# Kernel tuning notes

Measured on AMD Instinct MI355X. Metric: run time of the kernel, lower is better.

## Reference

```python
import jax, jax.numpy as jnp
import numpy as np

T, B = 128, 4096
TB = T * B
NUM_ACTIONS, N_WORDS, EMB = 6, 16, 16
IMG_FEAT, LOC_DIM, HID = 16, 4, 128
IN_DIM = IMG_FEAT + LOC_DIM + EMB  # 36
GRID_SIZE = 5.0


def setup_inputs() -> dict:
    key = jax.random.key(0)
    ks = jax.random.split(key, 32)
    p = lambda i, shape, s=0.1: (jax.random.normal(ks[i], shape, dtype=jnp.float32) * s)
    inp = {
        'image': jax.random.uniform(ks[0], (TB, 1, 3, 3), dtype=jnp.float32) * 255.0,
        'location': jax.random.uniform(ks[1], (TB, 2), dtype=jnp.float32) * GRID_SIZE,
        'message': jax.random.randint(ks[2], (TB,), 0, N_WORDS, dtype=jnp.int32),
        'done': (jax.random.uniform(ks[3], (TB,)) < 0.05).astype(jnp.float32),
        'h0': p(4, (B, HID)),
        'c0': p(5, (B, HID)),
        # visual encoder 9->256->256->128->16
        'vw1': p(6, (256, 9)), 'vb1': p(7, (256,)),
        'vw2': p(8, (256, 256)), 'vb2': p(9, (256,)),
        'vw3': p(10, (128, 256)), 'vb3': p(11, (128,)),
        'vw4': p(12, (IMG_FEAT, 128)), 'vb4': p(13, (IMG_FEAT,)),
        # message encoder: embedding + linear
        'emb': p(14, (N_WORDS, EMB)),
        'mw': p(15, (EMB, EMB)), 'mb': p(16, (EMB,)),
        # location encoder 2->4
        'lw': p(17, (LOC_DIM, 2)), 'lb': p(18, (LOC_DIM,)),
        # LSTM (PyTorch layout: gates ordered i,f,g,o)
        'w_ih': p(19, (4 * HID, IN_DIM)), 'w_hh': p(20, (4 * HID, HID)),
        'b_ih': p(21, (4 * HID,)), 'b_hh': p(22, (4 * HID,)),
        # heads
        'aw': p(23, (NUM_ACTIONS, HID), 0.01), 'ab': jnp.zeros((NUM_ACTIONS,), jnp.float32),
        'cw': p(24, (1, HID), 1.0), 'cb': jnp.zeros((1,), jnp.float32),
        'msw': p(25, (N_WORDS, HID), 0.01), 'msb': jnp.zeros((N_WORDS,), jnp.float32),
    }
    return inp


def _encode(image, location, message, vw1, vb1, vw2, vb2, vw3, vb3, vw4, vb4,
            emb, mw, mb, lw, lb):
    img = image.reshape(image.shape[0], -1) / 255.0  # [TB, 9]
    h = jax.nn.relu(img @ vw1.T + vb1)
    h = jax.nn.relu(h @ vw2.T + vb2)
    h = jax.nn.relu(h @ vw3.T + vb3)
    img_feat = jax.nn.relu(h @ vw4.T + vb4)           # [TB, 16]
    loc_feat = (location / GRID_SIZE) @ lw.T + lb     # [TB, 4]
    msg_feat = jax.nn.relu(emb[message] @ mw.T + mb)  # [TB, 16]
    return jnp.concatenate([img_feat, loc_feat, msg_feat], axis=1)  # [TB, 36]


def _lstm_scan(x, done, h0, c0, w_ih, w_hh, b_ih, b_hh):
    # x: [T, B, IN], done: [T, B]
    def step(carry, inp):
        h, c = carry
        xt, dt = inp
        mask = (1.0 - dt)[:, None]
        h = h * mask
        c = c * mask
        gates = xt @ w_ih.T + b_ih + h @ w_hh.T + b_hh  # [B, 4H]
        i, f, g, o = jnp.split(gates, 4, axis=1)
        i = jax.nn.sigmoid(i); f = jax.nn.sigmoid(f)
        g = jnp.tanh(g); o = jax.nn.sigmoid(o)
        c = f * c + i * g
        h = o * jnp.tanh(c)
        return (h, c), h
    (hN, cN), hs = jax.lax.scan(step, (h0, c0), (x, done))
    return hs, hN, cN


def reference(image, location, message, done, h0, c0,
              vw1, vb1, vw2, vb2, vw3, vb3, vw4, vb4,
              emb, mw, mb, lw, lb,
              w_ih, w_hh, b_ih, b_hh,
              aw, ab, cw, cb, msw, msb):
    feat = _encode(image, location, message, vw1, vb1, vw2, vb2, vw3, vb3,
                   vw4, vb4, emb, mw, mb, lw, lb)
    x = feat.reshape(T, B, IN_DIM)
    d = done.reshape(T, B)
    hs, hN, cN = _lstm_scan(x, d, h0, c0, w_ih, w_hh, b_ih, b_hh)
    hidden = hs.reshape(TB, HID)
    action_logits = hidden @ aw.T + ab    # [TB, num_actions]
    message_logits = hidden @ msw.T + msb  # [TB, n_words]
    value = hidden @ cw.T + cb            # [TB, 1]
    return hidden, action_logits, message_logits, value, hN, cN
```

## Files before the change

kernel.cpp:

```cpp
#include <hip/hip_runtime.h>
#include <hip/hip_fp16.h>

typedef _Float16 half8 __attribute__((ext_vector_type(8)));
typedef float f32x4 __attribute__((ext_vector_type(4)));

#define MFMA16(a, b, c) __builtin_amdgcn_mfma_f32_16x16x32_f16((a), (b), (c), 0, 0, 0)
#define DEVI __device__ __forceinline__

static constexpr int T_ = 128, B_ = 4096, HID_ = 128;
static constexpr int TB_ = T_ * B_;

static constexpr size_t W1P = 0;
static constexpr size_t W2P = 8192;
static constexpr size_t W3P = 73728;
static constexpr size_t W4P = 106496;
static constexpr size_t WHL = 108544;
static constexpr size_t MSGT = 305152;
static constexpr size_t FEAT = 305408;
static constexpr size_t WS_HALFS = FEAT + (size_t)TB_ * 40;

static constexpr size_t OUT_ACT = (size_t)TB_ * 128;
static constexpr size_t OUT_MSG = OUT_ACT + (size_t)TB_ * 6;
static constexpr size_t OUT_VAL = OUT_MSG + (size_t)TB_ * 16;
static constexpr size_t OUT_HN  = OUT_VAL + (size_t)TB_;
static constexpr size_t OUT_CN  = OUT_HN + (size_t)B_ * 128;

DEVI float sigm_(float x) { return __builtin_amdgcn_rcpf(1.f + __expf(-x)); }
DEVI float tanh_(float x) { return 1.f - 2.f * __builtin_amdgcn_rcpf(1.f + __expf(2.f * x)); }

DEVI void lds_barrier() {
    asm volatile("s_waitcnt lgkmcnt(0)" ::: "memory");
    __builtin_amdgcn_s_barrier();
    asm volatile("" ::: "memory");
}

DEVI void pack_one(const float* __restrict__ src, _Float16* __restrict__ dst,
                   int KT, int srcN, int srcK, int total, int idx) {
    if (idx >= total) return;
    int j = idx & 7, l = (idx >> 3) & 63, rest = idx >> 9;
    int kt = rest % KT, nt = rest / KT;
    int n = nt * 16 + (l & 15);
    int k = kt * 32 + ((l >> 4) << 3) + j;
    float v = (n < srcN && k < srcK) ? src[n * srcK + k] : 0.f;
    dst[idx] = (_Float16)v;
}

__global__ void k_prep(const float* __restrict__ vw1, const float* __restrict__ vw2,
                       const float* __restrict__ vw3, const float* __restrict__ vw4,
                       const float* __restrict__ wih, const float* __restrict__ whh,
                       const float* __restrict__ emb, const float* __restrict__ mw,
                       const float* __restrict__ mb, const float* __restrict__ bih,
                       const float* __restrict__ bhh, _Float16* __restrict__ wsh,
                       float* __restrict__ bcomb) {
    const int blk = blockIdx.x, tid = threadIdx.x;
    if (blk < 768) {
        int idx = blk * 256 + tid;
        int j = idx & 7, l = (idx >> 3) & 63, rest = idx >> 9;
        int kt = rest % 12, nt = rest / 12;
        int n = nt * 16 + (l & 15);
        int k = (kt % 6) * 32 + ((l >> 4) << 3) + j;
        float v;
        if (k < 64) v = (k < 36) ? wih[n * 36 + k] : 0.f;
        else        v = whh[n * 128 + (k - 64)];
        float hi = (float)(_Float16)v;
        wsh[WHL + idx] = (kt < 6) ? (_Float16)hi : (_Float16)(v - hi);
    } else if (blk < 800) {
        pack_one(vw1, wsh + W1P, 1, 256, 9, 8192, (blk - 768) * 256 + tid);
    } else if (blk < 1056) {
        pack_one(vw2, wsh + W2P, 8, 256, 256, 65536, (blk - 800) * 256 + tid);
    } else if (blk < 1184) {
        pack_one(vw3, wsh + W3P, 8, 128, 256, 32768, (blk - 1056) * 256 + tid);
    } else if (blk < 1192) {
        pack_one(vw4, wsh + W4P, 4, 16, 128, 2048, (blk - 1184) * 256 + tid);
    } else if (blk == 1192) {
        int w = tid >> 4, j = tid & 15;
        float a = mb[j];
        for (int e = 0; e < 16; ++e) a += emb[w * 16 + e] * mw[j * 16 + e];
        wsh[MSGT + tid] = (_Float16)fmaxf(a, 0.f);
    } else {
        int i = (blk - 1193) * 256 + tid;
        bcomb[i] = bih[i] + bhh[i];
    }
}

__global__ __launch_bounds__(256, 2)
void k_encoder(const float* __restrict__ img, const float* __restrict__ loc,
               const int* __restrict__ msg,
               const float* __restrict__ vb1, const float* __restrict__ vb2,
               const float* __restrict__ vb3, const float* __restrict__ vb4,
               const float* __restrict__ lw, const float* __restrict__ lb,
               const _Float16* __restrict__ wsh, _Float16* __restrict__ feat) {
    __shared__ __align__(16) _Float16 sA[64 * 40];
    __shared__ __align__(16) _Float16 sU[64 * 264];
    __shared__ __align__(16) _Float16 sV[64 * 264];
    __shared__ int smsg[64];

    const int tid = threadIdx.x;
    const int lane = tid & 63, wv = tid >> 6;
    const int lq = lane >> 4, lr = lane & 15;
    const int rowbase = blockIdx.x * 64;

    for (int i = tid; i < 576; i += 256) {
        int m = i / 9, k = i - m * 9;
        sA[m * 40 + k] = (_Float16)(img[(size_t)rowbase * 9 + i] * (1.f / 255.f));
    }
    for (int i = tid; i < 64 * 32; i += 256) {
        int m = i >> 5, k = 9 + (i & 31);
        if (k < 40) sA[m * 40 + k] = (_Float16)0.f;
    }
    if (tid < 64) smsg[tid] = msg[rowbase + tid];
    __syncthreads();

    const half8* w1p = (const half8*)(wsh + W1P);
    const half8* w2p = (const half8*)(wsh + W2P);
    const half8* w3p = (const half8*)(wsh + W3P);
    const half8* w4p = (const half8*)(wsh + W4P);

    {
        half8 afr[4];
        #pragma unroll
        for (int mt = 0; mt < 4; ++mt)
            afr[mt] = *(const half8*)&sA[(mt * 16 + lr) * 40 + lq * 8];
        #pragma unroll
        for (int ntl = 0; ntl < 4; ++ntl) {
            const int nt = wv * 4 + ntl;
            half8 bfr = w1p[nt * 64 + lane];
            f32x4 acc[4];
            #pragma unroll
            for (int mt = 0; mt < 4; ++mt) acc[mt] = (f32x4){0.f, 0.f, 0.f, 0.f};
            #pragma unroll
            for (int mt = 0; mt < 4; ++mt) acc[mt] = MFMA16(afr[mt], bfr, acc[mt]);
            const int n = nt * 16 + lr;
            const float bias = vb1[n];
            #pragma unroll
            for (int mt = 0; mt < 4; ++mt)
                #pragma unroll
                for (int r = 0; r < 4; ++r)
                    sU[(mt * 16 + lq * 4 + r) * 264 + n] = (_Float16)fmaxf(acc[mt][r] + bias, 0.f);
        }
    }
    __syncthreads();

    {
        half8 afr[4][8];
        #pragma unroll
        for (int mt = 0; mt < 4; ++mt)
            #pragma unroll
            for (int kt = 0; kt < 8; ++kt)
                afr[mt][kt] = *(const half8*)&sU[(mt * 16 + lr) * 264 + kt * 32 + lq * 8];
        #pragma unroll
        for (int ntl = 0; ntl < 4; ++ntl) {
            const int nt = wv * 4 + ntl;
            half8 bfr[8];
            #pragma unroll
            for (int kt = 0; kt < 8; ++kt) bfr[kt] = w2p[(nt * 8 + kt) * 64 + lane];
            f32x4 acc[4];
            #pragma unroll
            for (int mt = 0; mt < 4; ++mt) acc[mt] = (f32x4){0.f, 0.f, 0.f, 0.f};
            #pragma unroll
            for (int kt = 0; kt < 8; ++kt)
                #pragma unroll
                for (int mt = 0; mt < 4; ++mt)
                    acc[mt] = MFMA16(afr[mt][kt], bfr[kt], acc[mt]);
            const int n = nt * 16 + lr;
            const float bias = vb2[n];
            #pragma unroll
            for (int mt = 0; mt < 4; ++mt)
                #pragma unroll
                for (int r = 0; r < 4; ++r)
                    sV[(mt * 16 + lq * 4 + r) * 264 + n] = (_Float16)fmaxf(acc[mt][r] + bias, 0.f);
        }
    }
    __syncthreads();

    {
        half8 afr[4][8];
        #pragma unroll
        for (int mt = 0; mt < 4; ++mt)
            #pragma unroll
            for (int kt = 0; kt < 8; ++kt)
                afr[mt][kt] = *(const half8*)&sV[(mt * 16 + lr) * 264 + kt * 32 + lq * 8];
        #pragma unroll
        for (int ntl = 0; ntl < 2; ++ntl) {
            const int nt = wv * 2 + ntl;
            half8 bfr[8];
            #pragma unroll
            for (int kt = 0; kt < 8; ++kt) bfr[kt] = w3p[(nt * 8 + kt) * 64 + lane];
            f32x4 acc[4];
            #pragma unroll
            for (int mt = 0; mt < 4; ++mt) acc[mt] = (f32x4){0.f, 0.f, 0.f, 0.f};
            #pragma unroll
            for (int kt = 0; kt < 8; ++kt)
                #pragma unroll
                for (int mt = 0; mt < 4; ++mt)
                    acc[mt] = MFMA16(afr[mt][kt], bfr[kt], acc[mt]);
            const int n = nt * 16 + lr;
            const float bias = vb3[n];
            #pragma unroll
            for (int mt = 0; mt < 4; ++mt)
                #pragma unroll
                for (int r = 0; r < 4; ++r)
                    sU[(mt * 16 + lq * 4 + r) * 264 + n] = (_Float16)fmaxf(acc[mt][r] + bias, 0.f);
        }
    }
    __syncthreads();

    {
        half8 b4[4], a4[4];
        #pragma unroll
        for (int kt = 0; kt < 4; ++kt) {
            b4[kt] = w4p[kt * 64 + lane];
            a4[kt] = *(const half8*)&sU[(wv * 16 + lr) * 264 + kt * 32 + lq * 8];
        }
        f32x4 acc = (f32x4){0.f, 0.f, 0.f, 0.f};
        #pragma unroll
        for (int kt = 0; kt < 4; ++kt) acc = MFMA16(a4[kt], b4[kt], acc);
        const float bias = vb4[lr];
        #pragma unroll
        for (int r = 0; r < 4; ++r)
            sA[(wv * 16 + lq * 4 + r) * 40 + lr] = (_Float16)fmaxf(acc[r] + bias, 0.f);
    }

    {
        int m = tid >> 2, o = tid & 3;
        float x0 = loc[(size_t)(rowbase + m) * 2 + 0] * 0.2f;
        float x1 = loc[(size_t)(rowbase + m) * 2 + 1] * 0.2f;
        sA[m * 40 + 16 + o] = (_Float16)(x0 * lw[o * 2 + 0] + x1 * lw[o * 2 + 1] + lb[o]);
    }
    {
        const _Float16* mst = wsh + MSGT;
        for (int f = tid; f < 1024; f += 256) {
            int m = f >> 4, c = f & 15;
            sA[m * 40 + 20 + c] = mst[smsg[m] * 16 + c];
        }
    }
    {
        int m = tid >> 2, c = 36 + (tid & 3);
        sA[m * 40 + c] = (_Float16)0.f;
    }
    __syncthreads();

    uint4* dst = (uint4*)(feat + (size_t)rowbase * 40);
    const uint4* srcv = (const uint4*)sA;
    for (int i = tid; i < 320; i += 256) dst[i] = srcv[i];
}

__global__ __attribute__((amdgpu_flat_work_group_size(512, 512)))
__attribute__((amdgpu_waves_per_eu(2, 2)))
void k_lstm8(const _Float16* __restrict__ wsh, const float* __restrict__ bcomb,
             const float* __restrict__ done, const float* __restrict__ h0,
             const float* __restrict__ c0, float* __restrict__ hid,
             float* __restrict__ hN, float* __restrict__ cN) {
    __shared__ __align__(16) _Float16 sH[2][16 * 136];
    __shared__ __align__(16) _Float16 sX[2][16 * 72];
    __shared__ __align__(16) float sDm[2][16];

    const int tid = threadIdx.x;
    const int w = tid >> 6, lane = tid & 63;
    const int lq = lane >> 4, lr = lane & 15;
    const int b0 = blockIdx.x * 16;
    const int j = w * 16 + lr;
    const _Float16* feat = wsh + FEAT;
    const half8* wlt = (const half8*)(wsh + WHL);

    half8 wfr[4][12];
    #pragma unroll
    for (int g = 0; g < 4; ++g)
        #pragma unroll
        for (int kt = 0; kt < 12; ++kt)
            wfr[g][kt] = wlt[((8 * g + w) * 12 + kt) * 64 + lane];

    float bias[4];
    #pragma unroll
    for (int g = 0; g < 4; ++g) bias[g] = bcomb[g * 128 + j];

    f32x4 cc, hl;
    #pragma unroll
    for (int r = 0; r < 4; ++r) cc[r] = c0[(size_t)(b0 + lq * 4 + r) * 128 + j];

    for (int i = tid; i < 2048; i += 512) {
        int m = i >> 7, k = i & 127;
        sH[0][m * 136 + k] = (_Float16)h0[(size_t)(b0 + m) * 128 + k];
    }
    for (int i = tid; i < 1024; i += 512) {
        int bb = i >> 9, rem = i & 511;
        int m = rem >> 5, c = 40 + (rem & 31);
        sX[bb][m * 72 + c] = (_Float16)0.f;
    }
    const bool stx = tid < 160;
    const int sm = tid / 10, sc = tid - sm * 10;
    if (stx) *(uint2*)(&sX[0][sm * 72 + sc * 4]) =
        *(const uint2*)(feat + (size_t)(b0 + sm) * 40 + sc * 4);
    if (tid < 16) sDm[0][tid] = 1.f - done[b0 + tid];

    uint2 xrA = {0, 0}, xrB = {0, 0};
    float drA = 0.f, drB = 0.f;
    if (stx) xrA = *(const uint2*)(feat + ((size_t)B_ + b0 + sm) * 40 + sc * 4);
    if (tid < 16) drA = done[(size_t)B_ + b0 + tid];

    const _Float16* fptr = feat + ((size_t)2 * B_ + b0 + sm) * 40 + sc * 4;
    const float* dptr = done + (size_t)2 * B_ + b0 + tid;
    float* hq = hid + (size_t)b0 * 128 + j;

    __syncthreads();

    for (int t = 0; t < T_; ++t) {
        const int p = t & 1;
        const bool pf1 = (t + 1 < T_);
        const bool pf2 = (t + 2 < T_);

        if (stx && pf1) *(uint2*)(&sX[1 - p][sm * 72 + sc * 4]) = xrA;
        if (tid < 16 && pf1) sDm[1 - p][tid] = 1.f - drA;

        if (stx && pf2) xrB = *(const uint2*)fptr;
        if (tid < 16 && pf2) drB = dptr[0];
        fptr += (size_t)B_ * 40;
        dptr += B_;

        if (t > 0) {
            #pragma unroll
            for (int r = 0; r < 4; ++r)
                hq[(size_t)(lq * 4 + r) * 128] = hl[r];
            hq += (size_t)B_ * 128;
        }

        const f32x4 dmv = *(const f32x4*)&sDm[p][lq * 4];

        f32x4 acc[4];
        #pragma unroll
        for (int g = 0; g < 4; ++g) acc[g] = (f32x4){0.f, 0.f, 0.f, 0.f};
        #pragma unroll
        for (int u = 0; u < 4; ++u) {
            half8 av = *(const half8*)&sH[p][lr * 136 + u * 32 + lq * 8];
            #pragma unroll
            for (int g = 0; g < 4; ++g) acc[g] = MFMA16(av, wfr[g][2 + u], acc[g]);
            #pragma unroll
            for (int g = 0; g < 4; ++g) acc[g] = MFMA16(av, wfr[g][8 + u], acc[g]);
        }

        #pragma unroll
        for (int g = 0; g < 4; ++g)
            #pragma unroll
            for (int r = 0; r < 4; ++r)
                acc[g][r] = acc[g][r] * dmv[r] + bias[g];

        {
            half8 x0 = *(const half8*)&sX[p][lr * 72 + lq * 8];
            half8 x1 = *(const half8*)&sX[p][lr * 72 + 32 + lq * 8];
            #pragma unroll
            for (int g = 0; g < 4; ++g) acc[g] = MFMA16(x0, wfr[g][0], acc[g]);
            #pragma unroll
            for (int g = 0; g < 4; ++g) acc[g] = MFMA16(x0, wfr[g][6], acc[g]);
            #pragma unroll
            for (int g = 0; g < 4; ++g) acc[g] = MFMA16(x1, wfr[g][1], acc[g]);
            #pragma unroll
            for (int g = 0; g < 4; ++g) acc[g] = MFMA16(x1, wfr[g][7], acc[g]);
        }

        #pragma unroll
        for (int r = 0; r < 4; ++r) {
            const int m = lq * 4 + r;
            float iv = sigm_(acc[0][r]);
            float fv = sigm_(acc[1][r]);
            float gv = tanh_(acc[2][r]);
            float ov = sigm_(acc[3][r]);
            float cn = fv * (cc[r] * dmv[r]) + iv * gv;
            float hv = ov * tanh_(cn);
            cc[r] = cn;
            hl[r] = hv;
            sH[1 - p][m * 136 + j] = (_Float16)hv;
        }

        lds_barrier();
        xrA = xrB;
        drA = drB;
    }

    #pragma unroll
    for (int r = 0; r < 4; ++r) {
        hq[(size_t)(lq * 4 + r) * 128] = hl[r];
        hN[(size_t)(b0 + lq * 4 + r) * 128 + j] = hl[r];
        cN[(size_t)(b0 + lq * 4 + r) * 128 + j] = cc[r];
    }
}

__global__ __launch_bounds__(256)
void k_heads(const float* __restrict__ hidden, const float* __restrict__ aw,
             const float* __restrict__ ab, const float* __restrict__ cw,
             const float* __restrict__ cb, const float* __restrict__ msw,
             const float* __restrict__ msb, float* __restrict__ oact,
             float* __restrict__ omsg, float* __restrict__ oval) {
    __shared__ __align__(16) float sW[23 * 132];
    __shared__ float sWb[23];
    __shared__ __align__(16) float sHd[64 * 132];
    const int tid = threadIdx.x;
    const int rowbase = blockIdx.x * 64;

    for (int i = tid; i < 23 * 128; i += 256) {
        int o = i >> 7, k = i & 127;
        float v = (o < 6) ? aw[o * 128 + k] : (o < 22) ? msw[(o - 6) * 128 + k] : cw[k];
        sW[o * 132 + k] = v;
    }
    if (tid < 23) sWb[tid] = (tid < 6) ? ab[tid] : (tid < 22) ? msb[tid - 6] : cb[0];
    for (int i = tid; i < 8192; i += 256) {
        int m = i >> 7, k = i & 127;
        sHd[m * 132 + k] = hidden[(size_t)rowbase * 128 + i];
    }
    __syncthreads();

    for (int f = tid; f < 64 * 23; f += 256) {
        int m = f / 23, o = f - m * 23;
        const float* hp = &sHd[m * 132];
        const float* wp = &sW[o * 132];
        f32x4 av = (f32x4){0.f, 0.f, 0.f, 0.f};
        #pragma unroll
        for (int k = 0; k < 128; k += 4)
            av += (*(const f32x4*)(hp + k)) * (*(const f32x4*)(wp + k));
        float acc = sWb[o] + av[0] + av[1] + av[2] + av[3];
        int row = rowbase + m;
        if (o < 6)       oact[(size_t)row * 6 + o] = acc;
        else if (o < 22) omsg[(size_t)row * 16 + (o - 6)] = acc;
        else             oval[row] = acc;
    }
}

extern "C" void kernel_launch(void* const* d_in, const int* in_sizes, int n_in,
                              void* d_out, int out_size, void* d_ws, size_t ws_size,
                              hipStream_t stream) {
    const float* image = (const float*)d_in[0];
    const float* location = (const float*)d_in[1];
    const int*   message = (const int*)d_in[2];
    const float* done = (const float*)d_in[3];
    const float* h0 = (const float*)d_in[4];
    const float* c0 = (const float*)d_in[5];
    const float* vw1 = (const float*)d_in[6];  const float* vb1 = (const float*)d_in[7];
    const float* vw2 = (const float*)d_in[8];  const float* vb2 = (const float*)d_in[9];
    const float* vw3 = (const float*)d_in[10]; const float* vb3 = (const float*)d_in[11];
    const float* vw4 = (const float*)d_in[12]; const float* vb4 = (const float*)d_in[13];
    const float* emb = (const float*)d_in[14];
    const float* mw = (const float*)d_in[15];  const float* mb = (const float*)d_in[16];
    const float* lw = (const float*)d_in[17];  const float* lb = (const float*)d_in[18];
    const float* wih = (const float*)d_in[19]; const float* whh = (const float*)d_in[20];
    const float* bih = (const float*)d_in[21]; const float* bhh = (const float*)d_in[22];
    const float* aw = (const float*)d_in[23];  const float* ab = (const float*)d_in[24];
    const float* cw = (const float*)d_in[25];  const float* cb = (const float*)d_in[26];
    const float* msw = (const float*)d_in[27]; const float* msb = (const float*)d_in[28];

    _Float16* wsh = (_Float16*)d_ws;
    float* bcomb = (float*)((char*)d_ws + WS_HALFS * 2);

    float* out = (float*)d_out;
    float* oh   = out;
    float* oact = out + OUT_ACT;
    float* omsg = out + OUT_MSG;
    float* oval = out + OUT_VAL;
    float* ohN  = out + OUT_HN;
    float* ocN  = out + OUT_CN;

    k_prep<<<1195, 256, 0, stream>>>(vw1, vw2, vw3, vw4, wih, whh, emb, mw, mb,
                                     bih, bhh, wsh, bcomb);
    k_encoder<<<TB_ / 64, 256, 0, stream>>>(image, location, message, vb1, vb2, vb3, vb4,
                                            lw, lb, wsh, wsh + FEAT);
    k_lstm8<<<B_ / 16, 512, 0, stream>>>(wsh, bcomb, done, h0, c0, oh, ohN, ocN);
    k_heads<<<TB_ / 64, 256, 0, stream>>>(oh, aw, ab, cw, cb, msw, msb, oact, omsg, oval);
}
```

Baseline: 542.2 us.

## Fuse output heads into LSTM step using MFMA on fp16 hidden state

Removes the separate heads kernel. Two waves per LSTM block now compute action, message and value logits with MFMA from the fp16 hidden state already held in LDS, one step behind the recurrence, plus a tail step after the loop. This avoids re-reading the full fp32 hidden output and the extra launch, at the cost of more work on the serial LSTM critical path and fp16 precision for the heads. The two-step register prefetch of x and done is also reduced to a one-step load issued within the same iteration.

New measurement: 581.1 us. 1.07x slower.

```diff
diff --git a/kernel.cpp b/kernel.cpp
--- a/kernel.cpp
+++ b/kernel.cpp
@@ -16,7 +16,8 @@
 static constexpr size_t W4P = 106496;
 static constexpr size_t WHL = 108544;
 static constexpr size_t MSGT = 305152;
-static constexpr size_t FEAT = 305408;
+static constexpr size_t HDW = 305408;
+static constexpr size_t FEAT = 309504;
 static constexpr size_t WS_HALFS = FEAT + (size_t)TB_ * 40;
 
 static constexpr size_t OUT_ACT = (size_t)TB_ * 128;
@@ -27,12 +28,6 @@
 
 DEVI float sigm_(float x) { return __builtin_amdgcn_rcpf(1.f + __expf(-x)); }
 DEVI float tanh_(float x) { return 1.f - 2.f * __builtin_amdgcn_rcpf(1.f + __expf(2.f * x)); }
-
-DEVI void lds_barrier() {
-    asm volatile("s_waitcnt lgkmcnt(0)" ::: "memory");
-    __builtin_amdgcn_s_barrier();
-    asm volatile("" ::: "memory");
-}
 
 DEVI void pack_one(const float* __restrict__ src, _Float16* __restrict__ dst,
                    int KT, int srcN, int srcK, int total, int idx) {
@@ -50,8 +45,11 @@
                        const float* __restrict__ wih, const float* __restrict__ whh,
                        const float* __restrict__ emb, const float* __restrict__ mw,
                        const float* __restrict__ mb, const float* __restrict__ bih,
-                       const float* __restrict__ bhh, _Float16* __restrict__ wsh,
-                       float* __restrict__ bcomb) {
+                       const float* __restrict__ bhh,
+                       const float* __restrict__ aw, const float* __restrict__ ab,
+                       const float* __restrict__ cw, const float* __restrict__ cb,
+                       const float* __restrict__ msw, const float* __restrict__ msb,
+                       _Float16* __restrict__ wsh, float* __restrict__ bcomb) {
     const int blk = blockIdx.x, tid = threadIdx.x;
     if (blk < 768) {
         int idx = blk * 256 + tid;
@@ -77,9 +75,25 @@
         float a = mb[j];
         for (int e = 0; e < 16; ++e) a += emb[w * 16 + e] * mw[j * 16 + e];
         wsh[MSGT + tid] = (_Float16)fmaxf(a, 0.f);
-    } else {
+    } else if (blk < 1195) {
         int i = (blk - 1193) * 256 + tid;
         bcomb[i] = bih[i] + bhh[i];
+    } else if (blk < 1211) {
+        int idx = (blk - 1195) * 256 + tid;
+        int j = idx & 7, l = (idx >> 3) & 63, rest = idx >> 9;
+        int kt = rest & 3, nt = rest >> 2;
+        int n = nt * 16 + (l & 15);
+        int k = kt * 32 + ((l >> 4) << 3) + j;
+        float v = (n < 6) ? aw[n * 128 + k]
+                : (n < 22) ? msw[(n - 6) * 128 + k]
+                : (n == 22) ? cw[k] : 0.f;
+        wsh[HDW + idx] = (_Float16)v;
+    } else {
+        if (tid < 32) {
+            float* hb = bcomb + 512;
+            hb[tid] = (tid < 6) ? ab[tid] : (tid < 22) ? msb[tid - 6]
+                    : (tid == 22) ? cb[0] : 0.f;
+        }
     }
 }
 
@@ -250,7 +264,9 @@
 void k_lstm8(const _Float16* __restrict__ wsh, const float* __restrict__ bcomb,
              const float* __restrict__ done, const float* __restrict__ h0,
              const float* __restrict__ c0, float* __restrict__ hid,
-             float* __restrict__ hN, float* __restrict__ cN) {
+             float* __restrict__ hN, float* __restrict__ cN,
+             float* __restrict__ oact, float* __restrict__ omsg,
+             float* __restrict__ oval) {
     __shared__ __align__(16) _Float16 sH[2][16 * 136];
     __shared__ __align__(16) _Float16 sX[2][16 * 72];
     __shared__ __align__(16) float sDm[2][16];
@@ -274,6 +290,15 @@
     #pragma unroll
     for (int g = 0; g < 4; ++g) bias[g] = bcomb[g * 128 + j];
 
+    half8 hfr[4];
+    float hb0 = 0.f;
+    if (w < 2) {
+        const half8* hwp = (const half8*)(wsh + HDW);
+        #pragma unroll
+        for (int kt = 0; kt < 4; ++kt) hfr[kt] = hwp[(w * 4 + kt) * 64 + lane];
+        hb0 = (bcomb + 512)[w * 16 + lr];
+    }
+
     f32x4 cc, hl;
     #pragma unroll
     for (int r = 0; r < 4; ++r) cc[r] = c0[(size_t)(b0 + lq * 4 + r) * 128 + j];
@@ -292,28 +317,20 @@
     if (stx) *(uint2*)(&sX[0][sm * 72 + sc * 4]) =
         *(const uint2*)(feat + (size_t)(b0 + sm) * 40 + sc * 4);
     if (tid < 16) sDm[0][tid] = 1.f - done[b0 + tid];
-
-    uint2 xrA = {0, 0}, xrB = {0, 0};
-    float drA = 0.f, drB = 0.f;
-    if (stx) xrA = *(const uint2*)(feat + ((size_t)B_ + b0 + sm) * 40 + sc * 4);
-    if (tid < 16) drA = done[(size_t)B_ + b0 + tid];
-
-    const _Float16* fptr = feat + ((size_t)2 * B_ + b0 + sm) * 40 + sc * 4;
-    const float* dptr = done + (size_t)2 * B_ + b0 + tid;
+    __syncthreads();
+
+    const _Float16* fptr = feat + ((size_t)B_ + b0 + sm) * 40 + sc * 4;
+    const float* dptr = done + B_ + b0 + tid;
     float* hq = hid + (size_t)b0 * 128 + j;
-
-    __syncthreads();
 
     for (int t = 0; t < T_; ++t) {
         const int p = t & 1;
-        const bool pf1 = (t + 1 < T_);
-        const bool pf2 = (t + 2 < T_);
-
-        if (stx && pf1) *(uint2*)(&sX[1 - p][sm * 72 + sc * 4]) = xrA;
-        if (tid < 16 && pf1) sDm[1 - p][tid] = 1.f - drA;
-
-        if (stx && pf2) xrB = *(const uint2*)fptr;
-        if (tid < 16 && pf2) drB = dptr[0];
+        const bool pf = (t + 1 < T_);
+
+        uint2 xreg;
+        float dreg;
+        if (stx && pf) xreg = *(const uint2*)fptr;
+        if (tid < 16 && pf) dreg = dptr[0];
         fptr += (size_t)B_ * 40;
         dptr += B_;
 
@@ -326,17 +343,52 @@
 
         const f32x4 dmv = *(const f32x4*)&sDm[p][lq * 4];
 
+        half8 av0 = *(const half8*)&sH[p][lr * 136 + 0 * 32 + lq * 8];
+        half8 av1 = *(const half8*)&sH[p][lr * 136 + 1 * 32 + lq * 8];
+        half8 av2 = *(const half8*)&sH[p][lr * 136 + 2 * 32 + lq * 8];
+        half8 av3 = *(const half8*)&sH[p][lr * 136 + 3 * 32 + lq * 8];
         f32x4 acc[4];
         #pragma unroll
         for (int g = 0; g < 4; ++g) acc[g] = (f32x4){0.f, 0.f, 0.f, 0.f};
         #pragma unroll
-        for (int u = 0; u < 4; ++u) {
-            half8 av = *(const half8*)&sH[p][lr * 136 + u * 32 + lq * 8];
-            #pragma unroll
-            for (int g = 0; g < 4; ++g) acc[g] = MFMA16(av, wfr[g][2 + u], acc[g]);
-            #pragma unroll
-            for (int g = 0; g < 4; ++g) acc[g] = MFMA16(av, wfr[g][8 + u], acc[g]);
-        }
+        for (int g = 0; g < 4; ++g) acc[g] = MFMA16(av0, wfr[g][2], acc[g]);
+        #pragma unroll
+        for (int g = 0; g < 4; ++g) acc[g] = MFMA16(av0, wfr[g][8], acc[g]);
+        #pragma unroll
+        for (int g = 0; g < 4; ++g) acc[g] = MFMA16(av1, wfr[g][3], acc[g]);
+        #pragma unroll
+        for (int g = 0; g < 4; ++g) acc[g] = MFMA16(av1, wfr[g][9], acc[g]);
+        #pragma unroll
+        for (int g = 0; g < 4; ++g) acc[g] = MFMA16(av2, wfr[g][4], acc[g]);
+        #pragma unroll
+        for (int g = 0; g < 4; ++g) acc[g] = MFMA16(av2, wfr[g][10], acc[g]);
+        #pragma unroll
+        for (int g = 0; g < 4; ++g) acc[g] = MFMA16(av3, wfr[g][5], acc[g]);
+        #pragma unroll
+        for (int g = 0; g < 4; ++g) acc[g] = MFMA16(av3, wfr[g][11], acc[g]);
+
+        if (w < 2) {
+            f32x4 hacc = (f32x4){hb0, hb0, hb0, hb0};
+            hacc = MFMA16(av0, hfr[0], hacc);
+            hacc = MFMA16(av1, hfr[1], hacc);
+            hacc = MFMA16(av2, hfr[2], hacc);
+            hacc = MFMA16(av3, hfr[3], hacc);
+            if (t > 0) {
+                const size_t rbase = (size_t)(t - 1) * B_ + b0;
+                const int o = w * 16 + lr;
+                #pragma unroll
+                for (int r = 0; r < 4; ++r) {
+                    const size_t row = rbase + lq * 4 + r;
+                    float vv = hacc[r];
+                    if (o < 6)       oact[row * 6 + o] = vv;
+                    else if (o < 22) omsg[row * 16 + (o - 6)] = vv;
+                    else if (o == 22) oval[row] = vv;
+                }
+            }
+        }
+
+        if (stx && pf) *(uint2*)(&sX[1 - p][sm * 72 + sc * 4]) = xreg;
+        if (tid < 16 && pf) sDm[1 - p][tid] = 1.f - dreg;
 
         #pragma unroll
         for (int g = 0; g < 4; ++g)
@@ -371,9 +423,29 @@
             sH[1 - p][m * 136 + j] = (_Float16)hv;
         }
 
-        lds_barrier();
-        xrA = xrB;
-        drA = drB;
+        __syncthreads();
+    }
+
+    if (w < 2) {
+        half8 av0 = *(const half8*)&sH[0][lr * 136 + 0 * 32 + lq * 8];
+        half8 av1 = *(const half8*)&sH[0][lr * 136 + 1 * 32 + lq * 8];
+        half8 av2 = *(const half8*)&sH[0][lr * 136 + 2 * 32 + lq * 8];
+        half8 av3 = *(const half8*)&sH[0][lr * 136 + 3 * 32 + lq * 8];
+        f32x4 hacc = (f32x4){hb0, hb0, hb0, hb0};
+        hacc = MFMA16(av0, hfr[0], hacc);
+        hacc = MFMA16(av1, hfr[1], hacc);
+        hacc = MFMA16(av2, hfr[2], hacc);
+        hacc = MFMA16(av3, hfr[3], hacc);
+        const size_t rbase = (size_t)(T_ - 1) * B_ + b0;
+        const int o = w * 16 + lr;
+        #pragma unroll
+        for (int r = 0; r < 4; ++r) {
+            const size_t row = rbase + lq * 4 + r;
+            float vv = hacc[r];
+            if (o < 6)       oact[row * 6 + o] = vv;
+            else if (o < 22) omsg[row * 16 + (o - 6)] = vv;
+            else if (o == 22) oval[row] = vv;
+        }
     }
 
     #pragma unroll
@@ -381,46 +453,6 @@
         hq[(size_t)(lq * 4 + r) * 128] = hl[r];
         hN[(size_t)(b0 + lq * 4 + r) * 128 + j] = hl[r];
         cN[(size_t)(b0 + lq * 4 + r) * 128 + j] = cc[r];
-    }
-}
-
-__global__ __launch_bounds__(256)
-void k_heads(const float* __restrict__ hidden, const float* __restrict__ aw,
-             const float* __restrict__ ab, const float* __restrict__ cw,
-             const float* __restrict__ cb, const float* __restrict__ msw,
-             const float* __restrict__ msb, float* __restrict__ oact,
-             float* __restrict__ omsg, float* __restrict__ oval) {
-    __shared__ __align__(16) float sW[23 * 132];
-    __shared__ float sWb[23];
-    __shared__ __align__(16) float sHd[64 * 132];
-    const int tid = threadIdx.x;
-    const int rowbase = blockIdx.x * 64;
-
-    for (int i = tid; i < 23 * 128; i += 256) {
-        int o = i >> 7, k = i & 127;
-        float v = (o < 6) ? aw[o * 128 + k] : (o < 22) ? msw[(o - 6) * 128 + k] : cw[k];
-        sW[o * 132 + k] = v;
-    }
-    if (tid < 23) sWb[tid] = (tid < 6) ? ab[tid] : (tid < 22) ? msb[tid - 6] : cb[0];
-    for (int i = tid; i < 8192; i += 256) {
-        int m = i >> 7, k = i & 127;
-        sHd[m * 132 + k] = hidden[(size_t)rowbase * 128 + i];
-    }
-    __syncthreads();
-
-    for (int f = tid; f < 64 * 23; f += 256) {
-        int m = f / 23, o = f - m * 23;
-        const float* hp = &sHd[m * 132];
-        const float* wp = &sW[o * 132];
-        f32x4 av = (f32x4){0.f, 0.f, 0.f, 0.f};
-        #pragma unroll
-        for (int k = 0; k < 128; k += 4)
-            av += (*(const f32x4*)(hp + k)) * (*(const f32x4*)(wp + k));
-        float acc = sWb[o] + av[0] + av[1] + av[2] + av[3];
-        int row = rowbase + m;
-        if (o < 6)       oact[(size_t)row * 6 + o] = acc;
-        else if (o < 22) omsg[(size_t)row * 16 + (o - 6)] = acc;
-        else             oval[row] = acc;
     }
 }
 
@@ -457,10 +489,11 @@
     float* ohN  = out + OUT_HN;
     float* ocN  = out + OUT_CN;
 
-    k_prep<<<1195, 256, 0, stream>>>(vw1, vw2, vw3, vw4, wih, whh, emb, mw, mb,
-                                     bih, bhh, wsh, bcomb);
+    k_prep<<<1212, 256, 0, stream>>>(vw1, vw2, vw3, vw4, wih, whh, emb, mw, mb,
+                                     bih, bhh, aw, ab, cw, cb, msw, msb,
+                                     wsh, bcomb);
     k_encoder<<<TB_ / 64, 256, 0, stream>>>(image, location, message, vb1, vb2, vb3, vb4,
                                             lw, lb, wsh, wsh + FEAT);
-    k_lstm8<<<B_ / 16, 512, 0, stream>>>(wsh, bcomb, done, h0, c0, oh, ohN, ocN);
-    k_heads<<<TB_ / 64, 256, 0, stream>>>(oh, aw, ab, cw, cb, msw, msb, oact, omsg, oval);
+    k_lstm8<<<B_ / 16, 512, 0, stream>>>(wsh, bcomb, done, h0, c0, oh, ohN, ocN,
+                                         oact, omsg, oval);
 }
```
